# Kernel tuning notes

Hardware: AMD Instinct MI355X
Metric: run time of the kernel (lower is better)

The kernel has to match this reference:

```python
import jax, jax.numpy as jnp
import numpy as np

DEPTH_BINS = 64
TEMPERATURE = 1.0


def _conv2d(x, w, b, pad):
    y = jax.lax.conv_general_dilated(x, w, (1, 1), [(pad, pad), (pad, pad)],
                                     dimension_numbers=('NCHW', 'OIHW', 'NCHW'))
    return y + b[None, :, None, None]


def _conv3d(x, w, b, pad):
    y = jax.lax.conv_general_dilated(x, w, (1, 1, 1), [(pad, pad)] * 3,
                                     dimension_numbers=('NCDHW', 'OIDHW', 'NCDHW'))
    return y + b[None, :, None, None, None]


def setup_inputs() -> dict:
    key = jax.random.key(0)
    ks = jax.random.split(key, 16)
    B, N, C, H, W = 2, 5, 256, 96, 96
    s = 0.05  # weight scale
    return {
        'focal_features': jax.random.normal(ks[0], (B, N, C, H, W), jnp.float32),
        'focus_distances': jax.random.uniform(ks[1], (B, N), jnp.float32, 0.5, 5.0),
        'camera_encoding': jax.random.normal(ks[2], (B, 16), jnp.float32),
        'W1': jax.random.normal(ks[3], (256, 512, 3, 3), jnp.float32) * s,
        'b1': jnp.zeros((256,), jnp.float32),
        'W2': jax.random.normal(ks[4], (128, 256, 3, 3), jnp.float32) * s,
        'b2': jnp.zeros((128,), jnp.float32),
        'W3': jax.random.normal(ks[5], (1, 128, 1, 1), jnp.float32) * s,
        'b3': jnp.zeros((1,), jnp.float32),
        'R1': jax.random.normal(ks[6], (32, 64, 3, 3, 3), jnp.float32) * s,
        'rb1': jnp.zeros((32,), jnp.float32),
        'R2': jax.random.normal(ks[7], (16, 32, 3, 3, 3), jnp.float32) * s,
        'rb2': jnp.zeros((16,), jnp.float32),
        'R3': jax.random.normal(ks[8], (64, 16, 1, 1, 1), jnp.float32) * s,
        'rb3': jnp.zeros((64,), jnp.float32),
    }


def reference(focal_features, focus_distances, camera_encoding,
              W1, b1, W2, b2, W3, b3, R1, rb1, R2, rb2, R3, rb3):
    B, N, C, H, W = focal_features.shape
    # _apply_blur is identity and depth only affects the (unused) blur sigma,
    # so the per-depth matching cost is identical across all depth bins.
    feat_ref = focal_features[:, 0]  # [B,C,H,W]
    pair = jnp.concatenate(
        [focal_features, jnp.broadcast_to(feat_ref[:, None], focal_features.shape)],
        axis=2)  # [B,N,2C,H,W]
    x = pair.reshape(B * N, 2 * C, H, W)
    x = jax.nn.relu(_conv2d(x, W1, b1, 1))
    x = jax.nn.relu(_conv2d(x, W2, b2, 1))
    cost = _conv2d(x, W3, b3, 0)  # [B*N,1,H,W]
    cost_agg = cost.reshape(B, N, H, W).mean(axis=1)  # [B,H,W]
    # identical for every depth bin -> broadcast
    cv = jnp.broadcast_to(cost_agg[:, None], (B, DEPTH_BINS, H, W))
    # refine_net: Conv3d over channels=depth_bins, spatial dims (H, W, 1)
    v = cv[..., None]  # [B, depth_bins, H, W, 1]
    v = jax.nn.relu(_conv3d(v, R1, rb1, 1))
    v = jax.nn.relu(_conv3d(v, R2, rb2, 1))
    v = _conv3d(v, R3, rb3, 0)  # [B, depth_bins, H, W, 1]
    cv_ref = v[..., 0]  # [B, depth_bins, H, W]
    depth_probs = jax.nn.softmax(-cv_ref / TEMPERATURE, axis=1)
    cost_volume = jnp.transpose(cv_ref, (0, 2, 3, 1))   # [B,H,W,depth_bins]
    depth_probs = jnp.transpose(depth_probs, (0, 2, 3, 1))
    return cost_volume, depth_probs
```

## Files before the change

kernel.cpp:

```cpp
#include <hip/hip_runtime.h>
#include <stdint.h>

typedef unsigned short u16;
typedef _Float16 f16;
typedef _Float16 f16x8 __attribute__((ext_vector_type(8)));
typedef float    f32x4 __attribute__((ext_vector_type(4)));

#define HW   96
#define NPIX (HW*HW)
#define BBATCH 2
#define NVIEW  5
#define NIMG 10

#define LDS_B_OFF 6272
#define LDS_BYTES (6272 + 24576)

__device__ __forceinline__ int swz(int row, int chunk) {
    return ((row >> 1) << 7) + (((((row & 1) << 2) | chunk) ^ ((row >> 1) & 7)) << 4);
}

__device__ __forceinline__ u16 f16u(float f) {
    union { u16 u; f16 h; } v; v.h = (f16)f; return v.u;
}

__global__ __launch_bounds__(256)
void k_prep_w(const float* __restrict__ W1, const float* __restrict__ W2,
              const float* __restrict__ R1, const float* __restrict__ R2, const float* __restrict__ R3,
              u16* __restrict__ w1a, u16* __restrict__ w1b, u16* __restrict__ w2t,
              float* __restrict__ s1t, float* __restrict__ s2t, float* __restrict__ r3t)
{
    int id = blockIdx.x * 256 + threadIdx.x;
    if (id < 589824) {
        int t = id >> 16; int r = id & 65535; int o = r >> 8; int c = r & 255;
        int kh = t / 3, kw = t % 3;
        *(f16*)&w1a[id] = (f16)W1[((size_t)(o * 512 + c) * 3 + kh) * 3 + kw];
        *(f16*)&w1b[id] = (f16)W1[((size_t)(o * 512 + 256 + c) * 3 + kh) * 3 + kw];
        return;
    }
    id -= 589824;
    if (id < 294912) {
        int t = id >> 15; int r = id & 32767; int o = r >> 8; int c = r & 255;
        *(f16*)&w2t[id] = (f16)W2[((size_t)(o * 256 + c) * 3 + t / 3) * 3 + (t % 3)];
        return;
    }
    id -= 294912;
    if (id < 288) {
        int t = id >> 5; int o = id & 31;
        float s = 0.f;
        for (int i = 0; i < 64; ++i)
            s += R1[((size_t)((o * 64 + i) * 3 + t / 3) * 3 + t % 3) * 3 + 1];
        s1t[id] = s;
        return;
    }
    id -= 288;
    if (id < 4608) {
        int o = id & 15; int r = id >> 4; int i = r & 31; int t = r >> 5;
        s2t[id] = R2[((size_t)((o * 32 + i) * 3 + t / 3) * 3 + t % 3) * 3 + 1];
        return;
    }
    id -= 4608;
    if (id < 1024) {
        int o = id & 63; int i = id >> 6;
        r3t[id] = R3[(size_t)o * 16 + i];
    }
}

__global__ __launch_bounds__(256)
void k_tr(const float* __restrict__ src, u16* __restrict__ dst, int img0, int imgMul)
{
    const int cblk = blockIdx.x, row = blockIdx.y, z = blockIdx.z;
    const int gimg = img0 + z * imgMul;
    const int tid = threadIdx.x;
    __shared__ u16 tile[96 * 40];
    const int c = tid >> 3, j = tid & 7;
    const float* s = src + ((size_t)(gimg * 256 + cblk * 32 + c)) * NPIX + (size_t)row * HW + j * 12;
    #pragma unroll
    for (int k = 0; k < 3; ++k) {
        const float4 v = ((const float4*)s)[k];
        const int px = j * 12 + k * 4;
        tile[(px + 0) * 40 + c] = f16u(v.x);
        tile[(px + 1) * 40 + c] = f16u(v.y);
        tile[(px + 2) * 40 + c] = f16u(v.z);
        tile[(px + 3) * 40 + c] = f16u(v.w);
    }
    __syncthreads();
    if (tid < 192) {
        const int px = tid >> 1, part = tid & 1;
        const uint4 v0 = ((const uint4*)(tile + px * 40 + part * 16))[0];
        const uint4 v1 = ((const uint4*)(tile + px * 40 + part * 16))[1];
        uint4* d = (uint4*)(dst + ((((size_t)z * HW + row) * 8 + cblk) * HW + px) * 32 + part * 16);
        d[0] = v0; d[1] = v1;
    }
}

template<int MODE>
__global__ __launch_bounds__(256, 4)
void k_conv(const u16* __restrict__ in, const u16* __restrict__ wt,
            const u16* __restrict__ refp, const float* __restrict__ bias,
            const float* __restrict__ W3, void* __restrict__ outp, int ib)
{
    constexpr int Cout = (MODE == 2) ? 128 : 256;
    const int nwgY = gridDim.y;
    const int bid = blockIdx.x + HW * (blockIdx.y + nwgY * blockIdx.z);
    const int nwg = HW * nwgY * gridDim.z;
    const int wk  = (bid & 7) * (nwg >> 3) + (bid >> 3);
    const int h   = wk % HW;
    const int yz  = wk / HW;
    const int y   = yz % nwgY;
    const int ob  = (yz / nwgY) * 128;
    const int tid = threadIdx.x;
    const int wv = tid >> 6, l = tid & 63;
    const int wm = wv >> 1, wn = wv & 1;
    const int lane16 = l & 15, quad = l >> 4;

    __shared__ __align__(16) char lds[LDS_BYTES];

    f32x4 acc[3][4];
    #pragma unroll
    for (int mf = 0; mf < 3; ++mf)
        #pragma unroll
        for (int nf = 0; nf < 4; ++nf) acc[mf][nf] = (f32x4){0.f, 0.f, 0.f, 0.f};

    if (tid < 32) {
        const int base = (tid & 16) ? (48 * 128 + 64) : 0;
        ((unsigned int*)(lds + base))[tid & 15] = 0u;
    }

    for (int dh = -1; dh <= 1; ++dh) {
        const int hh = h + dh;
        if ((unsigned)hh >= (unsigned)HW) continue;
        for (int c0 = 0; c0 < 256; c0 += 32) {
            __syncthreads();
            if (tid < 192) {
                const int px = tid >> 1, half = tid & 1;
                const uint4* g = (const uint4*)(in +
                    ((((size_t)y * HW + hh) * 8 + (c0 >> 5)) * HW + px) * 32 + half * 16);
                const uint4 v0 = g[0], v1 = g[1];
                *(uint4*)(lds + swz(px + 1, half * 2))     = v0;
                *(uint4*)(lds + swz(px + 1, half * 2 + 1)) = v1;
            }
            #pragma unroll
            for (int i = 0; i < 3; ++i) {
                const int idx = i * 256 + tid;
                const int dwt = idx >> 8, o = (idx >> 1) & 127, half = idx & 1;
                const int tap = (dh + 1) * 3 + dwt;
                const uint4* g = (const uint4*)(wt +
                    ((size_t)tap * Cout + ob + o) * 256 + c0 + half * 16);
                const uint4 v0 = g[0], v1 = g[1];
                const int row = dwt * 128 + o;
                *(uint4*)(lds + LDS_B_OFF + swz(row, half * 2))     = v0;
                *(uint4*)(lds + LDS_B_OFF + swz(row, half * 2 + 1)) = v1;
            }
            __syncthreads();
            #pragma unroll
            for (int dw = 0; dw < 3; ++dw) {
                f16x8 af[3];
                #pragma unroll
                for (int mf = 0; mf < 3; ++mf)
                    af[mf] = *(const f16x8*)(lds + swz(wm * 48 + mf * 16 + lane16 + dw, quad));
                #pragma unroll
                for (int nf = 0; nf < 4; ++nf) {
                    const f16x8 bf = *(const f16x8*)(lds + LDS_B_OFF +
                        swz(dw * 128 + wn * 64 + nf * 16 + lane16, quad));
                    #pragma unroll
                    for (int mf = 0; mf < 3; ++mf)
                        acc[mf][nf] = __builtin_amdgcn_mfma_f32_16x16x32_f16(af[mf], bf, acc[mf][nf], 0, 0, 0);
                }
            }
        }
    }

    if (MODE <= 1) {
        const int rimg = (MODE == 1) ? (ib + y) / NVIEW : 0;
        float bias4[4] = {0.f, 0.f, 0.f, 0.f};
        if (MODE == 1) {
            #pragma unroll
            for (int nf = 0; nf < 4; ++nf) bias4[nf] = bias[ob + wn * 64 + nf * 16 + lane16];
        }
        char* epi = lds + wv * 3072;
        u16* outg = (u16*)outp;
        #pragma unroll
        for (int p = 0; p < 2; ++p) {
            __syncthreads();
            #pragma unroll
            for (int nn = 0; nn < 2; ++nn) {
                const int nf = p * 2 + nn;
                #pragma unroll
                for (int mf = 0; mf < 3; ++mf)
                    #pragma unroll
                    for (int r = 0; r < 4; ++r) {
                        const int pxl = mf * 16 + quad * 4 + r;
                        *(u16*)(epi + pxl * 64 + (nn * 16 + lane16) * 2) =
                            f16u(acc[mf][nf][r] + bias4[nf]);
                    }
            }
            __syncthreads();
            const int cblk = (ob + wn * 64 + p * 32) >> 5;
            const size_t obase = (((size_t)y * HW + h) * 8 + cblk) * (size_t)(HW * 32);
            const size_t rbase = (((size_t)rimg * HW + h) * 8 + cblk) * (size_t)(HW * 32);
            #pragma unroll
            for (int i = 0; i < 3; ++i) {
                const int u = i * 64 + l;
                const int pxl = u >> 2, part = u & 3;
                f16x8 v = *(const f16x8*)(epi + pxl * 64 + part * 16);
                const int px = wm * 48 + pxl;
                if (MODE == 1) {
                    const f16x8 rv = *(const f16x8*)(refp + rbase + (size_t)px * 32 + part * 8);
                    #pragma unroll
                    for (int jj = 0; jj < 8; ++jj)
                        v[jj] = (f16)fmaxf((float)v[jj] + (float)rv[jj], 0.f);
                }
                *(f16x8*)(outg + obase + (size_t)px * 32 + part * 8) = v;
            }
        }
    } else {
        const int gimg = ib + y;
        float w3v[4], b2v[4];
        #pragma unroll
        for (int nf = 0; nf < 4; ++nf) {
            const int o = wn * 64 + nf * 16 + lane16;
            w3v[nf] = W3[o]; b2v[nf] = bias[o];
        }
        float s[3][4];
        #pragma unroll
        for (int mf = 0; mf < 3; ++mf)
            #pragma unroll
            for (int r = 0; r < 4; ++r) {
                float t = 0.f;
                #pragma unroll
                for (int nf = 0; nf < 4; ++nf)
                    t += w3v[nf] * fmaxf(acc[mf][nf][r] + b2v[nf], 0.f);
                s[mf][r] = t;
            }
        #pragma unroll
        for (int xb = 1; xb < 16; xb <<= 1)
            #pragma unroll
            for (int mf = 0; mf < 3; ++mf)
                #pragma unroll
                for (int r = 0; r < 4; ++r)
                    s[mf][r] += __shfl_xor(s[mf][r], xb);
        __syncthreads();
        float* cs = (float*)lds;
        if (wn == 0 && lane16 == 0) {
            #pragma unroll
            for (int mf = 0; mf < 3; ++mf)
                #pragma unroll
                for (int r = 0; r < 4; ++r)
                    cs[wm * 48 + mf * 16 + quad * 4 + r] = s[mf][r];
        }
        __syncthreads();
        if (wn == 1 && lane16 == 0) {
            float* pvp = (float*)outp + (size_t)gimg * NPIX + (size_t)h * HW;
            #pragma unroll
            for (int mf = 0; mf < 3; ++mf)
                #pragma unroll
                for (int r = 0; r < 4; ++r) {
                    const int px = wm * 48 + mf * 16 + quad * 4 + r;
                    pvp[px] = cs[px] + s[mf][r];
                }
        }
    }
}

__global__ __launch_bounds__(256)
void k_cost_sum(const float* __restrict__ pv, const float* __restrict__ b3, float* __restrict__ ca)
{
    const int id = blockIdx.x * 256 + threadIdx.x;
    if (id >= BBATCH * NPIX) return;
    const int b = id / NPIX, hw = id % NPIX;
    float s = 0.f;
    #pragma unroll
    for (int n = 0; n < NVIEW; ++n) s += pv[(size_t)(b * NVIEW + n) * NPIX + hw];
    ca[id] = b3[0] + 0.2f * s;
}

__global__ __launch_bounds__(256)
void k_d1(const float* __restrict__ cost_agg, const float* __restrict__ s1t,
          const float* __restrict__ rb1, float* __restrict__ t1)
{
    const int id = blockIdx.x * 256 + threadIdx.x;
    const int o = id & 31; const int r = id >> 5;
    const int hw = r % NPIX; const int bimg = r / NPIX;
    const int y = hw / HW, x = hw % HW;
    const float* ca = cost_agg + (size_t)bimg * NPIX;
    float s = rb1[o];
    #pragma unroll
    for (int t = 0; t < 9; ++t) {
        const int yy = y + t / 3 - 1, xx = x + t % 3 - 1;
        if ((unsigned)yy < HW && (unsigned)xx < HW)
            s += s1t[t * 32 + o] * ca[yy * HW + xx];
    }
    t1[id] = fmaxf(s, 0.f);
}

__global__ __launch_bounds__(256)
void k_d2(const float* __restrict__ t1, const float* __restrict__ s2t,
          const float* __restrict__ rb2, float* __restrict__ t2)
{
    const int id = blockIdx.x * 256 + threadIdx.x;
    const int o = id & 15; const int r = id >> 4;
    const int hw = r % NPIX; const int bimg = r / NPIX;
    const int y = hw / HW, x = hw % HW;
    float s = rb2[o];
    for (int t = 0; t < 9; ++t) {
        const int yy = y + t / 3 - 1, xx = x + t % 3 - 1;
        if ((unsigned)yy < HW && (unsigned)xx < HW) {
            const float* tp = t1 + ((size_t)bimg * NPIX + yy * HW + xx) * 32;
            #pragma unroll
            for (int i = 0; i < 32; ++i)
                s += s2t[(t * 32 + i) * 16 + o] * tp[i];
        }
    }
    t2[id] = fmaxf(s, 0.f);
}

__global__ __launch_bounds__(256)
void k_d3(const float* __restrict__ t2, const float* __restrict__ r3t,
          const float* __restrict__ rb3, float* __restrict__ out)
{
    const int wv = threadIdx.x >> 6, o = threadIdx.x & 63;
    const int pix = blockIdx.x * 4 + wv;
    const float* tp = t2 + (size_t)pix * 16;
    float cv = rb3[o];
    #pragma unroll
    for (int i = 0; i < 16; ++i) cv += r3t[i * 64 + o] * tp[i];
    const float z = -cv;
    float m = z;
    #pragma unroll
    for (int off = 32; off; off >>= 1) m = fmaxf(m, __shfl_xor(m, off));
    const float e = __expf(z - m);
    float s = e;
    #pragma unroll
    for (int off = 32; off; off >>= 1) s += __shfl_xor(s, off);
    const float p = e / s;
    const size_t idx = (size_t)pix * 64 + o;
    out[idx] = cv;
    out[idx + (size_t)BBATCH * NPIX * 64] = p;
}

extern "C" void kernel_launch(void* const* d_in, const int* in_sizes, int n_in,
                              void* d_out, int out_size, void* d_ws, size_t ws_size,
                              hipStream_t stream)
{
    (void)in_sizes; (void)n_in; (void)out_size;
    const float* focal = (const float*)d_in[0];
    const float* W1  = (const float*)d_in[3];
    const float* b1  = (const float*)d_in[4];
    const float* W2  = (const float*)d_in[5];
    const float* b2  = (const float*)d_in[6];
    const float* W3  = (const float*)d_in[7];
    const float* b3  = (const float*)d_in[8];
    const float* R1  = (const float*)d_in[9];
    const float* rb1 = (const float*)d_in[10];
    const float* R2  = (const float*)d_in[11];
    const float* rb2 = (const float*)d_in[12];
    const float* R3  = (const float*)d_in[13];
    const float* rb3 = (const float*)d_in[14];

    char* ws = (char*)d_ws;
    size_t off = 0;
    auto alloc = [&](size_t sz) { char* p = ws + off; off = (off + sz + 255) & ~(size_t)255; return p; };
    const size_t IMG = (size_t)HW * 8 * HW * 32 * 2;
    u16*   w1a  = (u16*)  alloc(1179648);
    u16*   w1b  = (u16*)  alloc(1179648);
    u16*   w2t  = (u16*)  alloc(589824);
    float* s1t  = (float*)alloc(1152);
    float* s2t  = (float*)alloc(18432);
    float* r3t  = (float*)alloc(4096);
    float* ca   = (float*)alloc(73728);
    float* t1   = (float*)alloc(2359296);
    float* t2   = (float*)alloc(1179648);
    float* pv   = (float*)alloc(NIMG * NPIX * 4);
    u16*   refp   = (u16*)alloc(BBATCH * IMG);
    u16*   feats2 = (u16*)alloc(BBATCH * IMG);
    const size_t base = off;
    int C = 1;
    if (base + 20 * IMG + 512 <= ws_size)      C = 10;
    else if (base + 10 * IMG + 512 <= ws_size) C = 5;
    else if (base + 4 * IMG + 512 <= ws_size)  C = 2;
    u16* feats = (u16*)alloc((size_t)C * IMG);
    u16* x1    = (u16*)alloc((size_t)C * IMG);

    k_prep_w<<<(890656 + 255) / 256, 256, 0, stream>>>(W1, W2, R1, R2, R3, w1a, w1b, w2t, s1t, s2t, r3t);

    k_tr<<<dim3(8, HW, BBATCH), 256, 0, stream>>>(focal, feats2, 0, NVIEW);
    k_conv<0><<<dim3(HW, BBATCH, 2), 256, 0, stream>>>(feats2, w1b, nullptr, nullptr, nullptr, refp, 0);

    for (int ib = 0; ib < NIMG; ib += C) {
        k_tr<<<dim3(8, HW, C), 256, 0, stream>>>(focal, feats, ib, 1);
        k_conv<1><<<dim3(HW, C, 2), 256, 0, stream>>>(feats, w1a, refp, b1, nullptr, x1, ib);
        k_conv<2><<<dim3(HW, C, 1), 256, 0, stream>>>(x1, w2t, nullptr, b2, W3, pv, ib);
    }

    k_cost_sum<<<(BBATCH * NPIX + 255) / 256, 256, 0, stream>>>(pv, b3, ca);
    k_d1<<<(BBATCH * NPIX * 32) / 256, 256, 0, stream>>>(ca, s1t, rb1, t1);
    k_d2<<<(BBATCH * NPIX * 16) / 256, 256, 0, stream>>>(t1, s2t, rb2, t2);
    k_d3<<<(BBATCH * NPIX) / 4, 256, 0, stream>>>(t2, r3t, rb3, (float*)d_out);
}
```

Before: 457.8 us.

## Load conv weight fragments directly from global into registers, skipping LDS staging

Weights are pre-laid out in a channel-block-major, tap, output-channel layout so each lane can fetch its MFMA B fragments straight from global memory into registers, instead of staging them through shared memory. This removes the LDS writes and reads for the weight tile and shrinks LDS use to the activation tile. The launch bound occupancy hint drops from 4 to 3 to give room for the extra 12 fragment registers. The risk is that the weight loads now go to global or L2 on every iteration with no reuse across waves, and they sit on the critical path before the barrier.

```diff
diff --git a/kernel.cpp b/kernel.cpp
--- a/kernel.cpp
+++ b/kernel.cpp
@@ -12,8 +12,7 @@
 #define NVIEW  5
 #define NIMG 10
 
-#define LDS_B_OFF 6272
-#define LDS_BYTES (6272 + 24576)
+#define LDS_BYTES 12288
 
 __device__ __forceinline__ int swz(int row, int chunk) {
     return ((row >> 1) << 7) + (((((row & 1) << 2) | chunk) ^ ((row >> 1) & 7)) << 4);
@@ -33,14 +32,16 @@
     if (id < 589824) {
         int t = id >> 16; int r = id & 65535; int o = r >> 8; int c = r & 255;
         int kh = t / 3, kw = t % 3;
-        *(f16*)&w1a[id] = (f16)W1[((size_t)(o * 512 + c) * 3 + kh) * 3 + kw];
-        *(f16*)&w1b[id] = (f16)W1[((size_t)(o * 512 + 256 + c) * 3 + kh) * 3 + kw];
+        const int dst = (((c >> 5) * 9 + t) * 256 + o) * 32 + (c & 31);
+        *(f16*)&w1a[dst] = (f16)W1[((size_t)(o * 512 + c) * 3 + kh) * 3 + kw];
+        *(f16*)&w1b[dst] = (f16)W1[((size_t)(o * 512 + 256 + c) * 3 + kh) * 3 + kw];
         return;
     }
     id -= 589824;
     if (id < 294912) {
         int t = id >> 15; int r = id & 32767; int o = r >> 8; int c = r & 255;
-        *(f16*)&w2t[id] = (f16)W2[((size_t)(o * 256 + c) * 3 + t / 3) * 3 + (t % 3)];
+        const int dst = (((c >> 5) * 9 + t) * 128 + o) * 32 + (c & 31);
+        *(f16*)&w2t[dst] = (f16)W2[((size_t)(o * 256 + c) * 3 + t / 3) * 3 + (t % 3)];
         return;
     }
     id -= 294912;
@@ -94,7 +95,7 @@
 }
 
 template<int MODE>
-__global__ __launch_bounds__(256, 4)
+__global__ __launch_bounds__(256, 3)
 void k_conv(const u16* __restrict__ in, const u16* __restrict__ wt,
             const u16* __restrict__ refp, const float* __restrict__ bias,
             const float* __restrict__ W3, void* __restrict__ outp, int ib)
@@ -126,30 +127,34 @@
         ((unsigned int*)(lds + base))[tid & 15] = 0u;
     }
 
+    const u16* const wq = wt + (size_t)(ob + wn * 64 + lane16) * 32 + quad * 8;
+
     for (int dh = -1; dh <= 1; ++dh) {
         const int hh = h + dh;
         if ((unsigned)hh >= (unsigned)HW) continue;
+        const int tb = (dh + 1) * 3;
         for (int c0 = 0; c0 < 256; c0 += 32) {
             __syncthreads();
+            uint4 va0, va1;
             if (tid < 192) {
                 const int px = tid >> 1, half = tid & 1;
                 const uint4* g = (const uint4*)(in +
                     ((((size_t)y * HW + hh) * 8 + (c0 >> 5)) * HW + px) * 32 + half * 16);
-                const uint4 v0 = g[0], v1 = g[1];
-                *(uint4*)(lds + swz(px + 1, half * 2))     = v0;
-                *(uint4*)(lds + swz(px + 1, half * 2 + 1)) = v1;
-            }
-            #pragma unroll
-            for (int i = 0; i < 3; ++i) {
-                const int idx = i * 256 + tid;
-                const int dwt = idx >> 8, o = (idx >> 1) & 127, half = idx & 1;
-                const int tap = (dh + 1) * 3 + dwt;
-                const uint4* g = (const uint4*)(wt +
-                    ((size_t)tap * Cout + ob + o) * 256 + c0 + half * 16);
-                const uint4 v0 = g[0], v1 = g[1];
-                const int row = dwt * 128 + o;
-                *(uint4*)(lds + LDS_B_OFF + swz(row, half * 2))     = v0;
-                *(uint4*)(lds + LDS_B_OFF + swz(row, half * 2 + 1)) = v1;
+                va0 = g[0]; va1 = g[1];
+            }
+            f16x8 bf[12];
+            {
+                const u16* const ws = wq + (size_t)(((c0 >> 5) * 9 + tb) * Cout) * 32;
+                #pragma unroll
+                for (int dw = 0; dw < 3; ++dw)
+                    #pragma unroll
+                    for (int nf = 0; nf < 4; ++nf)
+                        bf[dw * 4 + nf] = *(const f16x8*)(ws + (dw * Cout + nf * 16) * 32);
+            }
+            if (tid < 192) {
+                const int px = tid >> 1, half = tid & 1;
+                *(uint4*)(lds + swz(px + 1, half * 2))     = va0;
+                *(uint4*)(lds + swz(px + 1, half * 2 + 1)) = va1;
             }
             __syncthreads();
             #pragma unroll
@@ -159,13 +164,10 @@
                 for (int mf = 0; mf < 3; ++mf)
                     af[mf] = *(const f16x8*)(lds + swz(wm * 48 + mf * 16 + lane16 + dw, quad));
                 #pragma unroll
-                for (int nf = 0; nf < 4; ++nf) {
-                    const f16x8 bf = *(const f16x8*)(lds + LDS_B_OFF +
-                        swz(dw * 128 + wn * 64 + nf * 16 + lane16, quad));
+                for (int nf = 0; nf < 4; ++nf)
                     #pragma unroll
                     for (int mf = 0; mf < 3; ++mf)
-                        acc[mf][nf] = __builtin_amdgcn_mfma_f32_16x16x32_f16(af[mf], bf, acc[mf][nf], 0, 0, 0);
-                }
+                        acc[mf][nf] = __builtin_amdgcn_mfma_f32_16x16x32_f16(af[mf], bf[dw * 4 + nf], acc[mf][nf], 0, 0, 0);
             }
         }
     }
```

New measurement: 489.7 us. 7.0% more time.
